# Performance work log

Measured on AMD Instinct MI355X. Metric: run time of the kernel, lower is better.

Reference implementation:

```python
import math
import jax, jax.numpy as jnp
import numpy as np

FS = 96000.0
N_BIQUADS = 16
HPF_FREQ_RANGE = (20.0, 500.0)
LPF_FREQ_RANGE = (5000.0, 20000.0)
SHELF_FREQ_RANGE = (50.0, 16000.0)
PEAK_FREQ_RANGE = (100.0, 15000.0)
Q_RANGE = (0.5, 16.0)
GAIN_RANGE = (-24.0, 24.0)
BROADBAND_RANGE = (-60.0, 0.0)


def _denorm_log(norm, lo, hi):
    return jnp.exp(math.log(lo) + norm * (math.log(hi) - math.log(lo)))


def _coef_highpass(fc, Q):
    w0 = 2.0 * math.pi * fc / FS
    alpha = jnp.sin(w0) / (2.0 * Q)
    c = jnp.cos(w0)
    b0 = (1 + c) / 2; b1 = -(1 + c); b2 = (1 + c) / 2
    a0 = 1 + alpha; a1 = -2 * c; a2 = 1 - alpha
    return b0 / a0, b1 / a0, b2 / a0, a1 / a0, a2 / a0


def _coef_lowpass(fc, Q):
    w0 = 2.0 * math.pi * fc / FS
    alpha = jnp.sin(w0) / (2.0 * Q)
    c = jnp.cos(w0)
    b0 = (1 - c) / 2; b1 = 1 - c; b2 = (1 - c) / 2
    a0 = 1 + alpha; a1 = -2 * c; a2 = 1 - alpha
    return b0 / a0, b1 / a0, b2 / a0, a1 / a0, a2 / a0


def _coef_lowshelf(fc, gain_db, Q):
    A = 10.0 ** (gain_db / 40.0)
    w0 = 2.0 * math.pi * fc / FS
    alpha = jnp.sin(w0) / (2.0 * Q)
    c = jnp.cos(w0)
    sA = jnp.sqrt(A)
    b0 = A * (A + 1 - (A - 1) * c + 2 * sA * alpha)
    b1 = 2 * A * (A - 1 - (A + 1) * c)
    b2 = A * (A + 1 - (A - 1) * c - 2 * sA * alpha)
    a0 = A + 1 + (A - 1) * c + 2 * sA * alpha
    a1 = -2 * (A - 1 + (A + 1) * c)
    a2 = A + 1 + (A - 1) * c - 2 * sA * alpha
    return b0 / a0, b1 / a0, b2 / a0, a1 / a0, a2 / a0


def _coef_highshelf(fc, gain_db, Q):
    A = 10.0 ** (gain_db / 40.0)
    w0 = 2.0 * math.pi * fc / FS
    alpha = jnp.sin(w0) / (2.0 * Q)
    c = jnp.cos(w0)
    sA = jnp.sqrt(A)
    b0 = A * (A + 1 + (A - 1) * c + 2 * sA * alpha)
    b1 = -2 * A * (A - 1 + (A + 1) * c)
    b2 = A * (A + 1 + (A - 1) * c - 2 * sA * alpha)
    a0 = A + 1 - (A - 1) * c + 2 * sA * alpha
    a1 = 2 * (A - 1 - (A + 1) * c)
    a2 = A + 1 - (A - 1) * c - 2 * sA * alpha
    return b0 / a0, b1 / a0, b2 / a0, a1 / a0, a2 / a0


def _coef_peak(fc, gain_db, Q):
    A = 10.0 ** (gain_db / 40.0)
    w0 = 2.0 * math.pi * fc / FS
    alpha = jnp.sin(w0) / (2.0 * Q)
    c = jnp.cos(w0)
    b0 = 1 + alpha * A; b1 = -2 * c; b2 = 1 - alpha * A
    a0 = 1 + alpha / A; a1 = -2 * c; a2 = 1 - alpha / A
    return b0 / a0, b1 / a0, b2 / a0, a1 / a0, a2 / a0


def _biquad(x, coefs):
    # x: (B, T); coefs: 5 arrays of shape (B,)
    b0, b1, b2, a1, a2 = coefs

    def step(carry, xt):  # xt: (B,)
        s1, s2 = carry
        y = b0 * xt + s1
        return (b1 * xt - a1 * y + s2, b2 * xt - a2 * y), y

    z = jnp.zeros(x.shape[0], x.dtype)
    _, ys = jax.lax.scan(step, (z, z), x.T)  # ys: (T, B)
    return ys.T


def _chain(audio, params):
    B = audio.shape[0]
    bp = params[:, :N_BIQUADS * 3].reshape(B, N_BIQUADS, 3)
    bb_lo, bb_hi = BROADBAND_RANGE
    in_db = bb_lo + params[:, -2] * (bb_hi - bb_lo)
    out_db = bb_lo + params[:, -1] * (bb_hi - bb_lo)
    x = audio * (10.0 ** (in_db / 20.0))[:, None]

    for i in range(N_BIQUADS):
        fn, gn, qn = bp[:, i, 0], bp[:, i, 1], bp[:, i, 2]
        Q = _denorm_log(qn, *Q_RANGE)
        gain = GAIN_RANGE[0] + gn * (GAIN_RANGE[1] - GAIN_RANGE[0])
        if i == 0:  # HPF
            coefs = _coef_highpass(_denorm_log(fn, *HPF_FREQ_RANGE), Q)
        elif i == 15:  # LPF
            coefs = _coef_lowpass(_denorm_log(fn, *LPF_FREQ_RANGE), Q)
        elif i == 1:  # low shelf
            coefs = _coef_lowshelf(_denorm_log(fn, *SHELF_FREQ_RANGE), gain, Q)
        elif i == 14:  # high shelf
            coefs = _coef_highshelf(_denorm_log(fn, *SHELF_FREQ_RANGE), gain, Q)
        else:  # peaking EQ
            coefs = _coef_peak(_denorm_log(fn, *PEAK_FREQ_RANGE), gain, Q)
        x = _biquad(x, coefs)

    return x * (10.0 ** (out_db / 20.0))[:, None]


def setup_inputs() -> dict:
    key = jax.random.key(0)
    k1, k2 = jax.random.split(key)
    audio = jax.random.normal(k1, (16, 262144), dtype=jnp.float32)
    params = jax.random.uniform(k2, (16, 50), dtype=jnp.float32)
    return {"audio": audio, "params": params}


def reference(audio, params):
    return _chain(audio, params)
```

## Files before the change

kernel.cpp:

```cpp
#include <hip/hip_runtime.h>
#include <math.h>

#define BATCH   16
#define T_LEN   262144
#define NB      16
#define L       64
#define GRP     64
#define SUB     16
#define CHAINS  4
#define NSUB    256
#define NSUP    16
#define NG      64
#define NCHUNK  4096

#define DPI 3.14159265358979323846264338327950288

#define OFF_COEF   0
#define OFF_A64    1536
#define OFF_A1K    17920
#define OFF_A16K   34304
#define OFF_QEND   50688
#define OFF_QSUP   181760
#define OFF_SSUP   189952
#define OFF_SARR   198144
#define OFF_P      329216

__device__ inline void stage_coefs(int i, double fn, double gn, double qn,
                                   double& B0, double& B1, double& B2,
                                   double& A1, double& A2) {
    const double FS = 96000.0;
    double Q    = exp(log(0.5) + qn * (log(16.0) - log(0.5)));
    double gain = -24.0 + gn * 48.0;
    double lo, hi;
    if (i == 0)            { lo = 20.0;   hi = 500.0;   }
    else if (i == 15)      { lo = 5000.0; hi = 20000.0; }
    else if (i == 1 || i == 14) { lo = 50.0; hi = 16000.0; }
    else                   { lo = 100.0;  hi = 15000.0; }
    double fc    = exp(log(lo) + fn * (log(hi) - log(lo)));
    double w0    = 2.0 * DPI * fc / FS;
    double alpha = sin(w0) / (2.0 * Q);
    double c     = cos(w0);
    double b0, b1, b2, a0, a1, a2;
    if (i == 0) {
        b0 = (1.0 + c) * 0.5; b1 = -(1.0 + c); b2 = (1.0 + c) * 0.5;
        a0 = 1.0 + alpha; a1 = -2.0 * c; a2 = 1.0 - alpha;
    } else if (i == 15) {
        b0 = (1.0 - c) * 0.5; b1 = 1.0 - c; b2 = (1.0 - c) * 0.5;
        a0 = 1.0 + alpha; a1 = -2.0 * c; a2 = 1.0 - alpha;
    } else if (i == 1) {
        double A = pow(10.0, gain / 40.0), sA = sqrt(A);
        b0 = A * ((A + 1.0) - (A - 1.0) * c + 2.0 * sA * alpha);
        b1 = 2.0 * A * ((A - 1.0) - (A + 1.0) * c);
        b2 = A * ((A + 1.0) - (A - 1.0) * c - 2.0 * sA * alpha);
        a0 = (A + 1.0) + (A - 1.0) * c + 2.0 * sA * alpha;
        a1 = -2.0 * ((A - 1.0) + (A + 1.0) * c);
        a2 = (A + 1.0) + (A - 1.0) * c - 2.0 * sA * alpha;
    } else if (i == 14) {
        double A = pow(10.0, gain / 40.0), sA = sqrt(A);
        b0 = A * ((A + 1.0) + (A - 1.0) * c + 2.0 * sA * alpha);
        b1 = -2.0 * A * ((A - 1.0) + (A + 1.0) * c);
        b2 = A * ((A + 1.0) + (A - 1.0) * c - 2.0 * sA * alpha);
        a0 = (A + 1.0) - (A - 1.0) * c + 2.0 * sA * alpha;
        a1 = 2.0 * ((A - 1.0) - (A + 1.0) * c);
        a2 = (A + 1.0) - (A - 1.0) * c - 2.0 * sA * alpha;
    } else {
        double A = pow(10.0, gain / 40.0);
        b0 = 1.0 + alpha * A; b1 = -2.0 * c; b2 = 1.0 - alpha * A;
        a0 = 1.0 + alpha / A; a1 = -2.0 * c; a2 = 1.0 - alpha / A;
    }
    B0 = b0 / a0; B1 = b1 / a0; B2 = b2 / a0; A1 = a1 / a0; A2 = a2 / a0;
}

__global__ __launch_bounds__(256) void k0_setup(const float* __restrict__ params,
                                                float* __restrict__ coefs,
                                                float* __restrict__ A64,
                                                float* __restrict__ A1K,
                                                float* __restrict__ A16K) {
    int b = blockIdx.x;
    int t = threadIdx.x;
    __shared__ double cf[NB][5];
    __shared__ double M1[32 * 32];
    __shared__ double M2[32 * 32];

    if (t < NB) {
        double B0, B1, B2, A1, A2;
        stage_coefs(t, (double)params[b * 50 + t * 3 + 0],
                       (double)params[b * 50 + t * 3 + 1],
                       (double)params[b * 50 + t * 3 + 2], B0, B1, B2, A1, A2);
        float f0 = (float)B0, f1 = (float)B1, f2 = (float)B2, f3 = (float)A1, f4 = (float)A2;
        cf[t][0] = (double)f0; cf[t][1] = (double)f1; cf[t][2] = (double)f2;
        cf[t][3] = (double)f3; cf[t][4] = (double)f4;
        float* cp = coefs + b * 96 + t * 5;
        cp[0] = f0; cp[1] = f1; cp[2] = f2; cp[3] = f3; cp[4] = f4;
    }
    if (t == NB) {
        double indb = -60.0 + (double)params[b * 50 + 48] * 60.0;
        coefs[b * 96 + 80] = (float)pow(10.0, indb / 20.0);
    }
    if (t == NB + 1) {
        double outdb = -60.0 + (double)params[b * 50 + 49] * 60.0;
        coefs[b * 96 + 81] = (float)pow(10.0, outdb / 20.0);
    }
    __syncthreads();

    if (t < 32) {
        double s1[NB], s2[NB];
#pragma unroll
        for (int i = 0; i < NB; i++) {
            s1[i] = (t == 2 * i) ? 1.0 : 0.0;
            s2[i] = (t == 2 * i + 1) ? 1.0 : 0.0;
        }
        double u = 0.0;
#pragma unroll
        for (int i = 0; i < NB; i++) {
            double y  = cf[i][0] * u + s1[i];
            double n1 = cf[i][1] * u - cf[i][3] * y + s2[i];
            double n2 = cf[i][2] * u - cf[i][4] * y;
            s1[i] = n1; s2[i] = n2; u = y;
        }
#pragma unroll
        for (int i = 0; i < NB; i++) {
            M1[(2 * i) * 32 + t]     = s1[i];
            M1[(2 * i + 1) * 32 + t] = s2[i];
        }
    }
    __syncthreads();

    int c  = t & 31;
    int r0 = t >> 5;
    double* src = M1;
    double* dst = M2;
    for (int sq = 0; sq < 14; sq++) {
        double acc[4] = {0.0, 0.0, 0.0, 0.0};
        for (int k = 0; k < 32; k++) {
            double bv = src[k * 32 + c];
#pragma unroll
            for (int e = 0; e < 4; e++)
                acc[e] += src[(e * 8 + r0) * 32 + k] * bv;
        }
#pragma unroll
        for (int e = 0; e < 4; e++) dst[(e * 8 + r0) * 32 + c] = acc[e];
        __syncthreads();
        { double* tmp = src; src = dst; dst = tmp; }
        float* out_m = (sq == 5) ? A64 : (sq == 9) ? A1K : (sq == 13) ? A16K : nullptr;
        if (out_m) {
#pragma unroll
            for (int e = 0; e < 4; e++) {
                int idx = (e * 8 + r0) * 32 + c;
                out_m[b * 1024 + idx] = (float)src[idx];
            }
        }
        __syncthreads();
    }
}

__global__ __launch_bounds__(64, 1) void k1_pass1(const float* __restrict__ audio,
                                                  const float* __restrict__ coefs,
                                                  const float* __restrict__ A64,
                                                  float* __restrict__ P,
                                                  float* __restrict__ Qend) {
    int blk   = blockIdx.x;
    int batch = blk >> 6;
    int grp   = blk & 63;
    int lane  = threadIdx.x;
    int chunk = grp * GRP + lane;

    const float* cf = coefs + batch * 96;
    float c0[NB], c1[NB], c2[NB], c3[NB], c4[NB];
#pragma unroll
    for (int i = 0; i < NB; i++) {
        c0[i] = cf[i * 5 + 0]; c1[i] = cf[i * 5 + 1]; c2[i] = cf[i * 5 + 2];
        c3[i] = cf[i * 5 + 3]; c4[i] = cf[i * 5 + 4];
    }
    float ing = cf[80];

    float s1[NB], s2[NB];
#pragma unroll
    for (int i = 0; i < NB; i++) { s1[i] = 0.f; s2[i] = 0.f; }

    const float4* xp = (const float4*)(audio + (size_t)batch * T_LEN + (size_t)chunk * L);
    float4 cur = xp[0];
    float4 nxt = xp[1];
#pragma unroll 1
    for (int tt = 0; tt < 16; tt++) {
        float4 fut = xp[(tt < 14) ? (tt + 2) : 15];
        float xs[4] = {cur.x, cur.y, cur.z, cur.w};
#pragma unroll
        for (int j = 0; j < 4; j++) {
            float u = ing * xs[j];
#pragma unroll
            for (int i = 0; i < NB; i++) {
                float y  = fmaf(c0[i], u, s1[i]);
                float n1 = fmaf(c1[i], u, s2[i]); n1 = fmaf(-c3[i], y, n1);
                float n2 = c2[i] * u;             n2 = fmaf(-c4[i], y, n2);
                s1[i] = n1; s2[i] = n2; u = y;
            }
        }
        cur = nxt; nxt = fut;
    }

    __shared__ float plds[GRP][33];
    float* pp = P + ((size_t)(batch * NCHUNK + chunk)) * 32;
#pragma unroll
    for (int i = 0; i < NB; i++) {
        float2 v; v.x = s1[i]; v.y = s2[i];
        *(float2*)(pp + 2 * i) = v;
        plds[lane][2 * i]     = s1[i];
        plds[lane][2 * i + 1] = s2[i];
    }
    __syncthreads();

    int row  = lane & 31;
    int half = lane >> 5;
    const float* alr = A64 + batch * 1024 + row * 32 + half * 16;
    float ar[16];
#pragma unroll
    for (int j = 0; j < 16; j++) ar[j] = alr[j];
    float q0 = 0.f, q1 = 0.f, q2 = 0.f, q3 = 0.f;
#pragma unroll 1
    for (int j = 0; j < SUB; j++) {
        float a0 = (half == 0) ? plds[0 * SUB + j][row] : 0.f;
        float a1 = (half == 0) ? plds[1 * SUB + j][row] : 0.f;
        float a2 = (half == 0) ? plds[2 * SUB + j][row] : 0.f;
        float a3 = (half == 0) ? plds[3 * SUB + j][row] : 0.f;
#pragma unroll
        for (int t = 0; t < 16; t++) {
            float w = ar[t];
            int src = half * 16 + t;
            a0 = fmaf(w, __shfl(q0, src, 64), a0);
            a1 = fmaf(w, __shfl(q1, src, 64), a1);
            a2 = fmaf(w, __shfl(q2, src, 64), a2);
            a3 = fmaf(w, __shfl(q3, src, 64), a3);
        }
        a0 += __shfl_xor(a0, 32, 64);
        a1 += __shfl_xor(a1, 32, 64);
        a2 += __shfl_xor(a2, 32, 64);
        a3 += __shfl_xor(a3, 32, 64);
        q0 = a0; q1 = a1; q2 = a2; q3 = a3;
    }
    if (lane < 32) {
        float* qe = Qend + ((size_t)(batch * NSUB + grp * CHAINS)) * 32 + row;
        qe[0 * 32] = q0; qe[1 * 32] = q1; qe[2 * 32] = q2; qe[3 * 32] = q3;
    }
}

__global__ __launch_bounds__(64, 1) void k2a(const float* __restrict__ A1K,
                                             const float* __restrict__ Qend,
                                             float* __restrict__ Qsup) {
    int batch = blockIdx.x >> 4;
    int sup   = blockIdx.x & 15;
    int lane  = threadIdx.x;
    int row   = lane & 31;
    int half  = lane >> 5;

    float pv[16];
#pragma unroll
    for (int j = 0; j < 16; j++)
        pv[j] = (half == 0) ? Qend[((size_t)(batch * NSUB + sup * 16 + j)) * 32 + row] : 0.f;

    const float* agr = A1K + batch * 1024 + row * 32 + half * 16;
    float ar[16];
#pragma unroll
    for (int j = 0; j < 16; j++) ar[j] = agr[j];

    float q = 0.f;
#pragma unroll 1
    for (int j = 0; j < 16; j++) {
        float acc = pv[j];
#pragma unroll
        for (int t = 0; t < 16; t++)
            acc = fmaf(ar[t], __shfl(q, half * 16 + t, 64), acc);
        acc += __shfl_xor(acc, 32, 64);
        q = acc;
    }
    if (lane < 32) Qsup[((size_t)(batch * NSUP + sup)) * 32 + row] = q;
}

__global__ __launch_bounds__(64, 1) void k2b(const float* __restrict__ A16K,
                                             const float* __restrict__ Qsup,
                                             float* __restrict__ Ssup) {
    int batch = blockIdx.x;
    int lane  = threadIdx.x;
    int row   = lane & 31;
    int half  = lane >> 5;

    float pv[16];
#pragma unroll
    for (int j = 0; j < 16; j++)
        pv[j] = (half == 0) ? Qsup[((size_t)(batch * NSUP + j)) * 32 + row] : 0.f;

    const float* agr = A16K + batch * 1024 + row * 32 + half * 16;
    float ar[16];
#pragma unroll
    for (int j = 0; j < 16; j++) ar[j] = agr[j];

    float S = 0.f;
#pragma unroll 1
    for (int s = 0; s < 16; s++) {
        if (lane < 32) Ssup[((size_t)(batch * NSUP + s)) * 32 + row] = S;
        float acc = pv[s];
#pragma unroll
        for (int t = 0; t < 16; t++)
            acc = fmaf(ar[t], __shfl(S, half * 16 + t, 64), acc);
        acc += __shfl_xor(acc, 32, 64);
        S = acc;
    }
}

__global__ __launch_bounds__(64, 1) void k2c(const float* __restrict__ A1K,
                                             const float* __restrict__ Qend,
                                             const float* __restrict__ Ssup,
                                             float* __restrict__ Sarr) {
    int batch = blockIdx.x >> 4;
    int sup   = blockIdx.x & 15;
    int lane  = threadIdx.x;
    int row   = lane & 31;
    int half  = lane >> 5;

    float pv[16];
#pragma unroll
    for (int j = 0; j < 16; j++)
        pv[j] = (half == 0) ? Qend[((size_t)(batch * NSUB + sup * 16 + j)) * 32 + row] : 0.f;

    const float* agr = A1K + batch * 1024 + row * 32 + half * 16;
    float ar[16];
#pragma unroll
    for (int j = 0; j < 16; j++) ar[j] = agr[j];

    float q = Ssup[((size_t)(batch * NSUP + sup)) * 32 + row];
#pragma unroll 1
    for (int j = 0; j < 16; j++) {
        if (lane < 32) Sarr[((size_t)(batch * NSUB + sup * 16 + j)) * 32 + row] = q;
        float acc = pv[j];
#pragma unroll
        for (int t = 0; t < 16; t++)
            acc = fmaf(ar[t], __shfl(q, half * 16 + t, 64), acc);
        acc += __shfl_xor(acc, 32, 64);
        q = acc;
    }
}

__global__ __launch_bounds__(64, 1) void k3_pass2(const float* __restrict__ audio,
                                                  const float* __restrict__ coefs,
                                                  const float* __restrict__ A64,
                                                  const float* __restrict__ P,
                                                  const float* __restrict__ Sarr,
                                                  float* __restrict__ out) {
    int blk   = blockIdx.x;
    int batch = blk >> 6;
    int grp   = blk & 63;
    int lane  = threadIdx.x;
    int chunk = grp * GRP + lane;

    __shared__ float plds[GRP][33];

    const float4* pp4 = (const float4*)(P + ((size_t)(batch * NCHUNK + chunk)) * 32);
#pragma unroll
    for (int r4 = 0; r4 < 8; r4++) {
        float4 v = pp4[r4];
        plds[lane][4 * r4 + 0] = v.x;
        plds[lane][4 * r4 + 1] = v.y;
        plds[lane][4 * r4 + 2] = v.z;
        plds[lane][4 * r4 + 3] = v.w;
    }
    __syncthreads();

    {
        int row  = lane & 31;
        int half = lane >> 5;
        const float* alr = A64 + batch * 1024 + row * 32 + half * 16;
        float ar[16];
#pragma unroll
        for (int j = 0; j < 16; j++) ar[j] = alr[j];
        const float* sp = Sarr + ((size_t)(batch * NSUB + grp * CHAINS)) * 32 + row;
        float q0 = sp[0 * 32], q1 = sp[1 * 32], q2 = sp[2 * 32], q3 = sp[3 * 32];
#pragma unroll 1
        for (int j = 0; j < SUB; j++) {
            float a0 = (half == 0) ? plds[0 * SUB + j][row] : 0.f;
            float a1 = (half == 0) ? plds[1 * SUB + j][row] : 0.f;
            float a2 = (half == 0) ? plds[2 * SUB + j][row] : 0.f;
            float a3 = (half == 0) ? plds[3 * SUB + j][row] : 0.f;
            if (half == 0) {
                plds[0 * SUB + j][row] = q0;
                plds[1 * SUB + j][row] = q1;
                plds[2 * SUB + j][row] = q2;
                plds[3 * SUB + j][row] = q3;
            }
#pragma unroll
            for (int t = 0; t < 16; t++) {
                float w = ar[t];
                int src = half * 16 + t;
                a0 = fmaf(w, __shfl(q0, src, 64), a0);
                a1 = fmaf(w, __shfl(q1, src, 64), a1);
                a2 = fmaf(w, __shfl(q2, src, 64), a2);
                a3 = fmaf(w, __shfl(q3, src, 64), a3);
            }
            a0 += __shfl_xor(a0, 32, 64);
            a1 += __shfl_xor(a1, 32, 64);
            a2 += __shfl_xor(a2, 32, 64);
            a3 += __shfl_xor(a3, 32, 64);
            q0 = a0; q1 = a1; q2 = a2; q3 = a3;
        }
    }
    __syncthreads();

    const float* cf = coefs + batch * 96;
    float c0[NB], c1[NB], c2[NB], c3[NB], c4[NB];
#pragma unroll
    for (int i = 0; i < NB; i++) {
        c0[i] = cf[i * 5 + 0]; c1[i] = cf[i * 5 + 1]; c2[i] = cf[i * 5 + 2];
        c3[i] = cf[i * 5 + 3]; c4[i] = cf[i * 5 + 4];
    }
    float ing  = cf[80];
    float outg = cf[81];

    float s1[NB], s2[NB];
#pragma unroll
    for (int i = 0; i < NB; i++) {
        s1[i] = plds[lane][2 * i];
        s2[i] = plds[lane][2 * i + 1];
    }

    const float4* xp = (const float4*)(audio + (size_t)batch * T_LEN + (size_t)chunk * L);
    float4* yp = (float4*)(out + (size_t)batch * T_LEN + (size_t)chunk * L);
    float4 cur = xp[0];
    float4 nxt = xp[1];
#pragma unroll 1
    for (int tt = 0; tt < 16; tt++) {
        float4 fut = xp[(tt < 14) ? (tt + 2) : 15];
        float xs[4] = {cur.x, cur.y, cur.z, cur.w};
        float ys[4];
#pragma unroll
        for (int j = 0; j < 4; j++) {
            float u = ing * xs[j];
#pragma unroll
            for (int i = 0; i < NB; i++) {
                float y  = fmaf(c0[i], u, s1[i]);
                float n1 = fmaf(c1[i], u, s2[i]); n1 = fmaf(-c3[i], y, n1);
                float n2 = c2[i] * u;             n2 = fmaf(-c4[i], y, n2);
                s1[i] = n1; s2[i] = n2; u = y;
            }
            ys[j] = outg * u;
        }
        float4 yv; yv.x = ys[0]; yv.y = ys[1]; yv.z = ys[2]; yv.w = ys[3];
        yp[tt] = yv;
        cur = nxt; nxt = fut;
    }
}

extern "C" void kernel_launch(void* const* d_in, const int* in_sizes, int n_in,
                              void* d_out, int out_size, void* d_ws, size_t ws_size,
                              hipStream_t stream) {
    const float* audio  = (const float*)d_in[0];
    const float* params = (const float*)d_in[1];
    float* out = (float*)d_out;
    float* ws  = (float*)d_ws;

    float* coefs = ws + OFF_COEF;
    float* A64   = ws + OFF_A64;
    float* A1K   = ws + OFF_A1K;
    float* A16K  = ws + OFF_A16K;
    float* Qend  = ws + OFF_QEND;
    float* Qsup  = ws + OFF_QSUP;
    float* Ssup  = ws + OFF_SSUP;
    float* Sarr  = ws + OFF_SARR;
    float* P     = ws + OFF_P;

    k0_setup<<<BATCH, 256, 0, stream>>>(params, coefs, A64, A1K, A16K);
    k1_pass1<<<BATCH * NG, 64, 0, stream>>>(audio, coefs, A64, P, Qend);
    k2a<<<BATCH * NSUP, 64, 0, stream>>>(A1K, Qend, Qsup);
    k2b<<<BATCH, 64, 0, stream>>>(A16K, Qsup, Ssup);
    k2c<<<BATCH * NSUP, 64, 0, stream>>>(A1K, Qend, Ssup, Sarr);
    k3_pass2<<<BATCH * NG, 64, 0, stream>>>(audio, coefs, A64, P, Sarr, out);
}
```

Before: 159.5 us.

## Fuse scan kernels into one cooperative kernel with grid syncs

Replaces the five post-setup kernels (pass1, three carry-propagation kernels, pass2) with a single cooperative kernel that uses grid.sync between phases. Per-chunk partial states stay in shared memory instead of going to a global P buffer, and the coefficients and A64 matrix are loaded once. This removes several kernel launch gaps and the P store/reload traffic. The cost is four grid-wide barriers, idle blocks during the small serial phases, and a requirement that all 1024 blocks be co-resident.

```diff
diff --git a/kernel.cpp b/kernel.cpp
--- a/kernel.cpp
+++ b/kernel.cpp
@@ -1,5 +1,8 @@
 #include <hip/hip_runtime.h>
+#include <hip/hip_cooperative_groups.h>
 #include <math.h>
+
+namespace cg = cooperative_groups;
 
 #define BATCH   16
 #define T_LEN   262144
@@ -15,15 +18,14 @@
 
 #define DPI 3.14159265358979323846264338327950288
 
-#define OFF_COEF   0
-#define OFF_A64    1536
-#define OFF_A1K    17920
-#define OFF_A16K   34304
-#define OFF_QEND   50688
-#define OFF_QSUP   181760
-#define OFF_SSUP   189952
-#define OFF_SARR   198144
-#define OFF_P      329216
+#define OFF_COEF  0
+#define OFF_A64   1536
+#define OFF_A1K   17920
+#define OFF_A16K  34304
+#define OFF_QEND  50688
+#define OFF_QSUP  181760
+#define OFF_SSUP  189952
+#define OFF_SARR  198144
 
 __device__ inline void stage_coefs(int i, double fn, double gn, double qn,
                                    double& B0, double& B1, double& B2,
@@ -154,16 +156,35 @@
     }
 }
 
-__global__ __launch_bounds__(64, 1) void k1_pass1(const float* __restrict__ audio,
-                                                  const float* __restrict__ coefs,
-                                                  const float* __restrict__ A64,
-                                                  float* __restrict__ P,
-                                                  float* __restrict__ Qend) {
+__device__ __forceinline__ float mv_step(const float* ar, float q, float addv, int half) {
+    float acc = addv;
+#pragma unroll
+    for (int t = 0; t < 16; t++)
+        acc = fmaf(ar[t], __shfl(q, half * 16 + t, 64), acc);
+    acc += __shfl_xor(acc, 32, 64);
+    return acc;
+}
+
+__global__ __launch_bounds__(64, 1) void mega(const float* __restrict__ audio,
+                                              const float* __restrict__ coefs,
+                                              const float* __restrict__ A64,
+                                              const float* __restrict__ A1K,
+                                              const float* __restrict__ A16K,
+                                              float* __restrict__ Qend,
+                                              float* __restrict__ Qsup,
+                                              float* __restrict__ Ssup,
+                                              float* __restrict__ Sarr,
+                                              float* __restrict__ out) {
+    cg::grid_group grid = cg::this_grid();
     int blk   = blockIdx.x;
     int batch = blk >> 6;
     int grp   = blk & 63;
     int lane  = threadIdx.x;
     int chunk = grp * GRP + lane;
+    int row   = lane & 31;
+    int half  = lane >> 5;
+
+    __shared__ float plds[GRP][33];
 
     const float* cf = coefs + batch * 96;
     float c0[NB], c1[NB], c2[NB], c3[NB], c4[NB];
@@ -172,208 +193,138 @@
         c0[i] = cf[i * 5 + 0]; c1[i] = cf[i * 5 + 1]; c2[i] = cf[i * 5 + 2];
         c3[i] = cf[i * 5 + 3]; c4[i] = cf[i * 5 + 4];
     }
-    float ing = cf[80];
-
-    float s1[NB], s2[NB];
-#pragma unroll
-    for (int i = 0; i < NB; i++) { s1[i] = 0.f; s2[i] = 0.f; }
-
-    const float4* xp = (const float4*)(audio + (size_t)batch * T_LEN + (size_t)chunk * L);
-    float4 cur = xp[0];
-    float4 nxt = xp[1];
-#pragma unroll 1
-    for (int tt = 0; tt < 16; tt++) {
-        float4 fut = xp[(tt < 14) ? (tt + 2) : 15];
-        float xs[4] = {cur.x, cur.y, cur.z, cur.w};
-#pragma unroll
-        for (int j = 0; j < 4; j++) {
-            float u = ing * xs[j];
-#pragma unroll
-            for (int i = 0; i < NB; i++) {
-                float y  = fmaf(c0[i], u, s1[i]);
-                float n1 = fmaf(c1[i], u, s2[i]); n1 = fmaf(-c3[i], y, n1);
-                float n2 = c2[i] * u;             n2 = fmaf(-c4[i], y, n2);
-                s1[i] = n1; s2[i] = n2; u = y;
-            }
-        }
-        cur = nxt; nxt = fut;
-    }
-
-    __shared__ float plds[GRP][33];
-    float* pp = P + ((size_t)(batch * NCHUNK + chunk)) * 32;
-#pragma unroll
-    for (int i = 0; i < NB; i++) {
-        float2 v; v.x = s1[i]; v.y = s2[i];
-        *(float2*)(pp + 2 * i) = v;
-        plds[lane][2 * i]     = s1[i];
-        plds[lane][2 * i + 1] = s2[i];
+    float ing  = cf[80];
+    float outg = cf[81];
+
+    float ar64[16];
+    {
+        const float* ap = A64 + batch * 1024 + row * 32 + half * 16;
+#pragma unroll
+        for (int j = 0; j < 16; j++) ar64[j] = ap[j];
+    }
+
+    {
+        float s1[NB], s2[NB];
+#pragma unroll
+        for (int i = 0; i < NB; i++) { s1[i] = 0.f; s2[i] = 0.f; }
+        const float4* xp = (const float4*)(audio + (size_t)batch * T_LEN + (size_t)chunk * L);
+        float4 a0v = xp[0];
+        float4 a1v = xp[1];
+#pragma unroll 1
+        for (int tt = 0; tt < 16; tt++) {
+            float4 fut = xp[(tt < 14) ? (tt + 2) : 15];
+            float xs[4] = {a0v.x, a0v.y, a0v.z, a0v.w};
+#pragma unroll
+            for (int j = 0; j < 4; j++) {
+                float u = ing * xs[j];
+#pragma unroll
+                for (int i = 0; i < NB; i++) {
+                    float y  = fmaf(c0[i], u, s1[i]);
+                    float n1 = fmaf(c1[i], u, s2[i]); n1 = fmaf(-c3[i], y, n1);
+                    float n2 = c2[i] * u;             n2 = fmaf(-c4[i], y, n2);
+                    s1[i] = n1; s2[i] = n2; u = y;
+                }
+            }
+            a0v = a1v; a1v = fut;
+        }
+#pragma unroll
+        for (int i = 0; i < NB; i++) {
+            plds[lane][2 * i]     = s1[i];
+            plds[lane][2 * i + 1] = s2[i];
+        }
     }
     __syncthreads();
-
-    int row  = lane & 31;
-    int half = lane >> 5;
-    const float* alr = A64 + batch * 1024 + row * 32 + half * 16;
-    float ar[16];
-#pragma unroll
-    for (int j = 0; j < 16; j++) ar[j] = alr[j];
-    float q0 = 0.f, q1 = 0.f, q2 = 0.f, q3 = 0.f;
-#pragma unroll 1
-    for (int j = 0; j < SUB; j++) {
-        float a0 = (half == 0) ? plds[0 * SUB + j][row] : 0.f;
-        float a1 = (half == 0) ? plds[1 * SUB + j][row] : 0.f;
-        float a2 = (half == 0) ? plds[2 * SUB + j][row] : 0.f;
-        float a3 = (half == 0) ? plds[3 * SUB + j][row] : 0.f;
-#pragma unroll
-        for (int t = 0; t < 16; t++) {
-            float w = ar[t];
-            int src = half * 16 + t;
-            a0 = fmaf(w, __shfl(q0, src, 64), a0);
-            a1 = fmaf(w, __shfl(q1, src, 64), a1);
-            a2 = fmaf(w, __shfl(q2, src, 64), a2);
-            a3 = fmaf(w, __shfl(q3, src, 64), a3);
-        }
-        a0 += __shfl_xor(a0, 32, 64);
-        a1 += __shfl_xor(a1, 32, 64);
-        a2 += __shfl_xor(a2, 32, 64);
-        a3 += __shfl_xor(a3, 32, 64);
-        q0 = a0; q1 = a1; q2 = a2; q3 = a3;
-    }
-    if (lane < 32) {
-        float* qe = Qend + ((size_t)(batch * NSUB + grp * CHAINS)) * 32 + row;
-        qe[0 * 32] = q0; qe[1 * 32] = q1; qe[2 * 32] = q2; qe[3 * 32] = q3;
-    }
-}
-
-__global__ __launch_bounds__(64, 1) void k2a(const float* __restrict__ A1K,
-                                             const float* __restrict__ Qend,
-                                             float* __restrict__ Qsup) {
-    int batch = blockIdx.x >> 4;
-    int sup   = blockIdx.x & 15;
-    int lane  = threadIdx.x;
-    int row   = lane & 31;
-    int half  = lane >> 5;
-
-    float pv[16];
-#pragma unroll
-    for (int j = 0; j < 16; j++)
-        pv[j] = (half == 0) ? Qend[((size_t)(batch * NSUB + sup * 16 + j)) * 32 + row] : 0.f;
-
-    const float* agr = A1K + batch * 1024 + row * 32 + half * 16;
-    float ar[16];
-#pragma unroll
-    for (int j = 0; j < 16; j++) ar[j] = agr[j];
-
-    float q = 0.f;
-#pragma unroll 1
-    for (int j = 0; j < 16; j++) {
-        float acc = pv[j];
-#pragma unroll
-        for (int t = 0; t < 16; t++)
-            acc = fmaf(ar[t], __shfl(q, half * 16 + t, 64), acc);
-        acc += __shfl_xor(acc, 32, 64);
-        q = acc;
-    }
-    if (lane < 32) Qsup[((size_t)(batch * NSUP + sup)) * 32 + row] = q;
-}
-
-__global__ __launch_bounds__(64, 1) void k2b(const float* __restrict__ A16K,
-                                             const float* __restrict__ Qsup,
-                                             float* __restrict__ Ssup) {
-    int batch = blockIdx.x;
-    int lane  = threadIdx.x;
-    int row   = lane & 31;
-    int half  = lane >> 5;
-
-    float pv[16];
-#pragma unroll
-    for (int j = 0; j < 16; j++)
-        pv[j] = (half == 0) ? Qsup[((size_t)(batch * NSUP + j)) * 32 + row] : 0.f;
-
-    const float* agr = A16K + batch * 1024 + row * 32 + half * 16;
-    float ar[16];
-#pragma unroll
-    for (int j = 0; j < 16; j++) ar[j] = agr[j];
-
-    float S = 0.f;
-#pragma unroll 1
-    for (int s = 0; s < 16; s++) {
-        if (lane < 32) Ssup[((size_t)(batch * NSUP + s)) * 32 + row] = S;
-        float acc = pv[s];
-#pragma unroll
-        for (int t = 0; t < 16; t++)
-            acc = fmaf(ar[t], __shfl(S, half * 16 + t, 64), acc);
-        acc += __shfl_xor(acc, 32, 64);
-        S = acc;
-    }
-}
-
-__global__ __launch_bounds__(64, 1) void k2c(const float* __restrict__ A1K,
-                                             const float* __restrict__ Qend,
-                                             const float* __restrict__ Ssup,
-                                             float* __restrict__ Sarr) {
-    int batch = blockIdx.x >> 4;
-    int sup   = blockIdx.x & 15;
-    int lane  = threadIdx.x;
-    int row   = lane & 31;
-    int half  = lane >> 5;
-
-    float pv[16];
-#pragma unroll
-    for (int j = 0; j < 16; j++)
-        pv[j] = (half == 0) ? Qend[((size_t)(batch * NSUB + sup * 16 + j)) * 32 + row] : 0.f;
-
-    const float* agr = A1K + batch * 1024 + row * 32 + half * 16;
-    float ar[16];
-#pragma unroll
-    for (int j = 0; j < 16; j++) ar[j] = agr[j];
-
-    float q = Ssup[((size_t)(batch * NSUP + sup)) * 32 + row];
-#pragma unroll 1
-    for (int j = 0; j < 16; j++) {
-        if (lane < 32) Sarr[((size_t)(batch * NSUB + sup * 16 + j)) * 32 + row] = q;
-        float acc = pv[j];
-#pragma unroll
-        for (int t = 0; t < 16; t++)
-            acc = fmaf(ar[t], __shfl(q, half * 16 + t, 64), acc);
-        acc += __shfl_xor(acc, 32, 64);
-        q = acc;
-    }
-}
-
-__global__ __launch_bounds__(64, 1) void k3_pass2(const float* __restrict__ audio,
-                                                  const float* __restrict__ coefs,
-                                                  const float* __restrict__ A64,
-                                                  const float* __restrict__ P,
-                                                  const float* __restrict__ Sarr,
-                                                  float* __restrict__ out) {
-    int blk   = blockIdx.x;
-    int batch = blk >> 6;
-    int grp   = blk & 63;
-    int lane  = threadIdx.x;
-    int chunk = grp * GRP + lane;
-
-    __shared__ float plds[GRP][33];
-
-    const float4* pp4 = (const float4*)(P + ((size_t)(batch * NCHUNK + chunk)) * 32);
-#pragma unroll
-    for (int r4 = 0; r4 < 8; r4++) {
-        float4 v = pp4[r4];
-        plds[lane][4 * r4 + 0] = v.x;
-        plds[lane][4 * r4 + 1] = v.y;
-        plds[lane][4 * r4 + 2] = v.z;
-        plds[lane][4 * r4 + 3] = v.w;
-    }
-    __syncthreads();
-
     {
-        int row  = lane & 31;
-        int half = lane >> 5;
-        const float* alr = A64 + batch * 1024 + row * 32 + half * 16;
-        float ar[16];
-#pragma unroll
-        for (int j = 0; j < 16; j++) ar[j] = alr[j];
+        float q0 = 0.f, q1 = 0.f, q2 = 0.f, q3 = 0.f;
+#pragma unroll 1
+        for (int j = 0; j < SUB; j++) {
+            float a0 = (half == 0) ? plds[0 * SUB + j][row] : 0.f;
+            float a1 = (half == 0) ? plds[1 * SUB + j][row] : 0.f;
+            float a2 = (half == 0) ? plds[2 * SUB + j][row] : 0.f;
+            float a3 = (half == 0) ? plds[3 * SUB + j][row] : 0.f;
+#pragma unroll
+            for (int t = 0; t < 16; t++) {
+                float w = ar64[t];
+                int src = half * 16 + t;
+                a0 = fmaf(w, __shfl(q0, src, 64), a0);
+                a1 = fmaf(w, __shfl(q1, src, 64), a1);
+                a2 = fmaf(w, __shfl(q2, src, 64), a2);
+                a3 = fmaf(w, __shfl(q3, src, 64), a3);
+            }
+            a0 += __shfl_xor(a0, 32, 64);
+            a1 += __shfl_xor(a1, 32, 64);
+            a2 += __shfl_xor(a2, 32, 64);
+            a3 += __shfl_xor(a3, 32, 64);
+            q0 = a0; q1 = a1; q2 = a2; q3 = a3;
+        }
+        if (lane < 32) {
+            float* qe = Qend + ((size_t)(batch * NSUB + grp * CHAINS)) * 32 + row;
+            qe[0] = q0; qe[32] = q1; qe[64] = q2; qe[96] = q3;
+        }
+    }
+
+    __threadfence();
+    grid.sync();
+
+    float ar1k[16];
+    if (grp < 16) {
+        int sup = grp;
+        const float* ap = A1K + batch * 1024 + row * 32 + half * 16;
+#pragma unroll
+        for (int j = 0; j < 16; j++) ar1k[j] = ap[j];
+        float pv[16];
+#pragma unroll
+        for (int j = 0; j < 16; j++)
+            pv[j] = (half == 0) ? Qend[((size_t)(batch * NSUB + sup * 16 + j)) * 32 + row] : 0.f;
+        float q = 0.f;
+#pragma unroll 1
+        for (int j = 0; j < 16; j++) q = mv_step(ar1k, q, pv[j], half);
+        if (lane < 32) Qsup[((size_t)(batch * NSUP + sup)) * 32 + row] = q;
+    }
+
+    __threadfence();
+    grid.sync();
+
+    if (grp == 0) {
+        float ark[16];
+        const float* ap = A16K + batch * 1024 + row * 32 + half * 16;
+#pragma unroll
+        for (int j = 0; j < 16; j++) ark[j] = ap[j];
+        float pv[16];
+#pragma unroll
+        for (int j = 0; j < 16; j++)
+            pv[j] = (half == 0) ? Qsup[((size_t)(batch * NSUP + j)) * 32 + row] : 0.f;
+        float S = 0.f;
+#pragma unroll 1
+        for (int s = 0; s < 16; s++) {
+            if (lane < 32) Ssup[((size_t)(batch * NSUP + s)) * 32 + row] = S;
+            S = mv_step(ark, S, pv[s], half);
+        }
+    }
+
+    __threadfence();
+    grid.sync();
+
+    if (grp < 16) {
+        int sup = grp;
+        float pv[16];
+#pragma unroll
+        for (int j = 0; j < 16; j++)
+            pv[j] = (half == 0) ? Qend[((size_t)(batch * NSUB + sup * 16 + j)) * 32 + row] : 0.f;
+        float q = Ssup[((size_t)(batch * NSUP + sup)) * 32 + row];
+#pragma unroll 1
+        for (int j = 0; j < 16; j++) {
+            if (lane < 32) Sarr[((size_t)(batch * NSUB + sup * 16 + j)) * 32 + row] = q;
+            q = mv_step(ar1k, q, pv[j], half);
+        }
+    }
+
+    __threadfence();
+    grid.sync();
+
+    {
         const float* sp = Sarr + ((size_t)(batch * NSUB + grp * CHAINS)) * 32 + row;
-        float q0 = sp[0 * 32], q1 = sp[1 * 32], q2 = sp[2 * 32], q3 = sp[3 * 32];
+        float q0 = sp[0], q1 = sp[32], q2 = sp[64], q3 = sp[96];
 #pragma unroll 1
         for (int j = 0; j < SUB; j++) {
             float a0 = (half == 0) ? plds[0 * SUB + j][row] : 0.f;
@@ -388,7 +339,7 @@
             }
 #pragma unroll
             for (int t = 0; t < 16; t++) {
-                float w = ar[t];
+                float w = ar64[t];
                 int src = half * 16 + t;
                 a0 = fmaf(w, __shfl(q0, src, 64), a0);
                 a1 = fmaf(w, __shfl(q1, src, 64), a1);
@@ -404,47 +355,38 @@
     }
     __syncthreads();
 
-    const float* cf = coefs + batch * 96;
-    float c0[NB], c1[NB], c2[NB], c3[NB], c4[NB];
-#pragma unroll
-    for (int i = 0; i < NB; i++) {
-        c0[i] = cf[i * 5 + 0]; c1[i] = cf[i * 5 + 1]; c2[i] = cf[i * 5 + 2];
-        c3[i] = cf[i * 5 + 3]; c4[i] = cf[i * 5 + 4];
-    }
-    float ing  = cf[80];
-    float outg = cf[81];
-
-    float s1[NB], s2[NB];
-#pragma unroll
-    for (int i = 0; i < NB; i++) {
-        s1[i] = plds[lane][2 * i];
-        s2[i] = plds[lane][2 * i + 1];
-    }
-
-    const float4* xp = (const float4*)(audio + (size_t)batch * T_LEN + (size_t)chunk * L);
-    float4* yp = (float4*)(out + (size_t)batch * T_LEN + (size_t)chunk * L);
-    float4 cur = xp[0];
-    float4 nxt = xp[1];
-#pragma unroll 1
-    for (int tt = 0; tt < 16; tt++) {
-        float4 fut = xp[(tt < 14) ? (tt + 2) : 15];
-        float xs[4] = {cur.x, cur.y, cur.z, cur.w};
-        float ys[4];
-#pragma unroll
-        for (int j = 0; j < 4; j++) {
-            float u = ing * xs[j];
-#pragma unroll
-            for (int i = 0; i < NB; i++) {
-                float y  = fmaf(c0[i], u, s1[i]);
-                float n1 = fmaf(c1[i], u, s2[i]); n1 = fmaf(-c3[i], y, n1);
-                float n2 = c2[i] * u;             n2 = fmaf(-c4[i], y, n2);
-                s1[i] = n1; s2[i] = n2; u = y;
-            }
-            ys[j] = outg * u;
-        }
-        float4 yv; yv.x = ys[0]; yv.y = ys[1]; yv.z = ys[2]; yv.w = ys[3];
-        yp[tt] = yv;
-        cur = nxt; nxt = fut;
+    {
+        float s1[NB], s2[NB];
+#pragma unroll
+        for (int i = 0; i < NB; i++) {
+            s1[i] = plds[lane][2 * i];
+            s2[i] = plds[lane][2 * i + 1];
+        }
+        const float4* xp = (const float4*)(audio + (size_t)batch * T_LEN + (size_t)chunk * L);
+        float4* yp = (float4*)(out + (size_t)batch * T_LEN + (size_t)chunk * L);
+        float4 a0v = xp[0];
+        float4 a1v = xp[1];
+#pragma unroll 1
+        for (int tt = 0; tt < 16; tt++) {
+            float4 fut = xp[(tt < 14) ? (tt + 2) : 15];
+            float xs[4] = {a0v.x, a0v.y, a0v.z, a0v.w};
+            float ys[4];
+#pragma unroll
+            for (int j = 0; j < 4; j++) {
+                float u = ing * xs[j];
+#pragma unroll
+                for (int i = 0; i < NB; i++) {
+                    float y  = fmaf(c0[i], u, s1[i]);
+                    float n1 = fmaf(c1[i], u, s2[i]); n1 = fmaf(-c3[i], y, n1);
+                    float n2 = c2[i] * u;             n2 = fmaf(-c4[i], y, n2);
+                    s1[i] = n1; s2[i] = n2; u = y;
+                }
+                ys[j] = outg * u;
+            }
+            float4 yv; yv.x = ys[0]; yv.y = ys[1]; yv.z = ys[2]; yv.w = ys[3];
+            yp[tt] = yv;
+            a0v = a1v; a1v = fut;
+        }
     }
 }
 
@@ -464,12 +406,16 @@
     float* Qsup  = ws + OFF_QSUP;
     float* Ssup  = ws + OFF_SSUP;
     float* Sarr  = ws + OFF_SARR;
-    float* P     = ws + OFF_P;
 
     k0_setup<<<BATCH, 256, 0, stream>>>(params, coefs, A64, A1K, A16K);
-    k1_pass1<<<BATCH * NG, 64, 0, stream>>>(audio, coefs, A64, P, Qend);
-    k2a<<<BATCH * NSUP, 64, 0, stream>>>(A1K, Qend, Qsup);
-    k2b<<<BATCH, 64, 0, stream>>>(A16K, Qsup, Ssup);
-    k2c<<<BATCH * NSUP, 64, 0, stream>>>(A1K, Qend, Ssup, Sarr);
-    k3_pass2<<<BATCH * NG, 64, 0, stream>>>(audio, coefs, A64, P, Sarr, out);
+
+    const float* c_coefs = coefs;
+    const float* c_A64   = A64;
+    const float* c_A1K   = A1K;
+    const float* c_A16K  = A16K;
+    void* args[] = {(void*)&audio, (void*)&c_coefs, (void*)&c_A64, (void*)&c_A1K,
+                    (void*)&c_A16K, (void*)&Qend, (void*)&Qsup, (void*)&Ssup,
+                    (void*)&Sarr, (void*)&out};
+    hipLaunchCooperativeKernel((const void*)mega, dim3(BATCH * NG), dim3(64),
+                               args, 0, stream);
 }
```

Measured after the change: 626.3 us. 293% more time.

## Fuse three state-combine kernels into one block per batch and coalesce P layout

Applied to the files above, without the earlier changes.

Replaces the three small combine kernels (k2a, k2b, k2c) with one 256-thread kernel per batch. Each of its four waves handles four superchunk chains, exchanging intermediate states through shared memory with block barriers, which removes two kernel launches and their global round trips. The per-chunk state buffer P is also changed to a lane-contiguous layout so stores in pass1 and loads in pass2 are coalesced. In exchange, the combine step now runs on only 16 blocks with more serial work per wave instead of 256 parallel blocks.

```diff
diff --git a/kernel.cpp b/kernel.cpp
--- a/kernel.cpp
+++ b/kernel.cpp
@@ -15,15 +15,13 @@
 
 #define DPI 3.14159265358979323846264338327950288
 
-#define OFF_COEF   0
-#define OFF_A64    1536
-#define OFF_A1K    17920
-#define OFF_A16K   34304
-#define OFF_QEND   50688
-#define OFF_QSUP   181760
-#define OFF_SSUP   189952
-#define OFF_SARR   198144
-#define OFF_P      329216
+#define OFF_COEF  0
+#define OFF_A64   1536
+#define OFF_A1K   17920
+#define OFF_A16K  34304
+#define OFF_QEND  50688
+#define OFF_SARR  181760
+#define OFF_P     312832
 
 __device__ inline void stage_coefs(int i, double fn, double gn, double qn,
                                    double& B0, double& B1, double& B2,
@@ -154,6 +152,15 @@
     }
 }
 
+__device__ __forceinline__ float mv_step(const float* ar, float q, float addv, int half) {
+    float acc = addv;
+#pragma unroll
+    for (int t = 0; t < 16; t++)
+        acc = fmaf(ar[t], __shfl(q, half * 16 + t, 64), acc);
+    acc += __shfl_xor(acc, 32, 64);
+    return acc;
+}
+
 __global__ __launch_bounds__(64, 1) void k1_pass1(const float* __restrict__ audio,
                                                   const float* __restrict__ coefs,
                                                   const float* __restrict__ A64,
@@ -199,12 +206,18 @@
         cur = nxt; nxt = fut;
     }
 
+    {
+        float* pb = P + ((size_t)(batch * NG + grp)) * 2048;
+#pragma unroll
+        for (int i = 0; i < NB; i++) {
+            pb[(2 * i) * 64 + lane]     = s1[i];
+            pb[(2 * i + 1) * 64 + lane] = s2[i];
+        }
+    }
+
     __shared__ float plds[GRP][33];
-    float* pp = P + ((size_t)(batch * NCHUNK + chunk)) * 32;
 #pragma unroll
     for (int i = 0; i < NB; i++) {
-        float2 v; v.x = s1[i]; v.y = s2[i];
-        *(float2*)(pp + 2 * i) = v;
         plds[lane][2 * i]     = s1[i];
         plds[lane][2 * i + 1] = s2[i];
     }
@@ -240,103 +253,116 @@
     }
     if (lane < 32) {
         float* qe = Qend + ((size_t)(batch * NSUB + grp * CHAINS)) * 32 + row;
-        qe[0 * 32] = q0; qe[1 * 32] = q1; qe[2 * 32] = q2; qe[3 * 32] = q3;
-    }
-}
-
-__global__ __launch_bounds__(64, 1) void k2a(const float* __restrict__ A1K,
-                                             const float* __restrict__ Qend,
-                                             float* __restrict__ Qsup) {
-    int batch = blockIdx.x >> 4;
-    int sup   = blockIdx.x & 15;
-    int lane  = threadIdx.x;
+        qe[0] = q0; qe[32] = q1; qe[64] = q2; qe[96] = q3;
+    }
+}
+
+__global__ __launch_bounds__(256, 1) void k2_combine(const float* __restrict__ A1K,
+                                                     const float* __restrict__ A16K,
+                                                     const float* __restrict__ Qend,
+                                                     float* __restrict__ Sarr) {
+    int batch = blockIdx.x;
+    int tid   = threadIdx.x;
+    int wave  = tid >> 6;
+    int lane  = tid & 63;
     int row   = lane & 31;
     int half  = lane >> 5;
 
-    float pv[16];
-#pragma unroll
-    for (int j = 0; j < 16; j++)
-        pv[j] = (half == 0) ? Qend[((size_t)(batch * NSUB + sup * 16 + j)) * 32 + row] : 0.f;
-
-    const float* agr = A1K + batch * 1024 + row * 32 + half * 16;
-    float ar[16];
-#pragma unroll
-    for (int j = 0; j < 16; j++) ar[j] = agr[j];
-
-    float q = 0.f;
-#pragma unroll 1
-    for (int j = 0; j < 16; j++) {
-        float acc = pv[j];
-#pragma unroll
-        for (int t = 0; t < 16; t++)
-            acc = fmaf(ar[t], __shfl(q, half * 16 + t, 64), acc);
-        acc += __shfl_xor(acc, 32, 64);
-        q = acc;
-    }
-    if (lane < 32) Qsup[((size_t)(batch * NSUP + sup)) * 32 + row] = q;
-}
-
-__global__ __launch_bounds__(64, 1) void k2b(const float* __restrict__ A16K,
-                                             const float* __restrict__ Qsup,
-                                             float* __restrict__ Ssup) {
-    int batch = blockIdx.x;
-    int lane  = threadIdx.x;
-    int row   = lane & 31;
-    int half  = lane >> 5;
-
-    float pv[16];
-#pragma unroll
-    for (int j = 0; j < 16; j++)
-        pv[j] = (half == 0) ? Qsup[((size_t)(batch * NSUP + j)) * 32 + row] : 0.f;
-
-    const float* agr = A16K + batch * 1024 + row * 32 + half * 16;
-    float ar[16];
-#pragma unroll
-    for (int j = 0; j < 16; j++) ar[j] = agr[j];
-
-    float S = 0.f;
-#pragma unroll 1
-    for (int s = 0; s < 16; s++) {
-        if (lane < 32) Ssup[((size_t)(batch * NSUP + s)) * 32 + row] = S;
-        float acc = pv[s];
-#pragma unroll
-        for (int t = 0; t < 16; t++)
-            acc = fmaf(ar[t], __shfl(S, half * 16 + t, 64), acc);
-        acc += __shfl_xor(acc, 32, 64);
-        S = acc;
-    }
-}
-
-__global__ __launch_bounds__(64, 1) void k2c(const float* __restrict__ A1K,
-                                             const float* __restrict__ Qend,
-                                             const float* __restrict__ Ssup,
-                                             float* __restrict__ Sarr) {
-    int batch = blockIdx.x >> 4;
-    int sup   = blockIdx.x & 15;
-    int lane  = threadIdx.x;
-    int row   = lane & 31;
-    int half  = lane >> 5;
-
-    float pv[16];
-#pragma unroll
-    for (int j = 0; j < 16; j++)
-        pv[j] = (half == 0) ? Qend[((size_t)(batch * NSUB + sup * 16 + j)) * 32 + row] : 0.f;
-
-    const float* agr = A1K + batch * 1024 + row * 32 + half * 16;
-    float ar[16];
-#pragma unroll
-    for (int j = 0; j < 16; j++) ar[j] = agr[j];
-
-    float q = Ssup[((size_t)(batch * NSUP + sup)) * 32 + row];
-#pragma unroll 1
-    for (int j = 0; j < 16; j++) {
-        if (lane < 32) Sarr[((size_t)(batch * NSUB + sup * 16 + j)) * 32 + row] = q;
-        float acc = pv[j];
-#pragma unroll
-        for (int t = 0; t < 16; t++)
-            acc = fmaf(ar[t], __shfl(q, half * 16 + t, 64), acc);
-        acc += __shfl_xor(acc, 32, 64);
-        q = acc;
+    __shared__ float qe[NSUB][32];
+    __shared__ float qs[NSUP][32];
+    __shared__ float ss[NSUP][32];
+
+    {
+        const float4* src4 = (const float4*)(Qend + (size_t)batch * NSUB * 32);
+        float4* dst4 = (float4*)&qe[0][0];
+        for (int i = tid; i < NSUB * 32 / 4; i += 256) dst4[i] = src4[i];
+    }
+    float ar1k[16];
+    {
+        const float* ap = A1K + batch * 1024 + row * 32 + half * 16;
+#pragma unroll
+        for (int j = 0; j < 16; j++) ar1k[j] = ap[j];
+    }
+    __syncthreads();
+
+    int s0i = wave * 4;
+    {
+        float q0 = 0.f, q1 = 0.f, q2 = 0.f, q3 = 0.f;
+#pragma unroll 1
+        for (int j = 0; j < 16; j++) {
+            float a0 = (half == 0) ? qe[(s0i + 0) * 16 + j][row] : 0.f;
+            float a1 = (half == 0) ? qe[(s0i + 1) * 16 + j][row] : 0.f;
+            float a2 = (half == 0) ? qe[(s0i + 2) * 16 + j][row] : 0.f;
+            float a3 = (half == 0) ? qe[(s0i + 3) * 16 + j][row] : 0.f;
+#pragma unroll
+            for (int t = 0; t < 16; t++) {
+                float w = ar1k[t];
+                int src = half * 16 + t;
+                a0 = fmaf(w, __shfl(q0, src, 64), a0);
+                a1 = fmaf(w, __shfl(q1, src, 64), a1);
+                a2 = fmaf(w, __shfl(q2, src, 64), a2);
+                a3 = fmaf(w, __shfl(q3, src, 64), a3);
+            }
+            a0 += __shfl_xor(a0, 32, 64);
+            a1 += __shfl_xor(a1, 32, 64);
+            a2 += __shfl_xor(a2, 32, 64);
+            a3 += __shfl_xor(a3, 32, 64);
+            q0 = a0; q1 = a1; q2 = a2; q3 = a3;
+        }
+        if (lane < 32) {
+            qs[s0i + 0][row] = q0; qs[s0i + 1][row] = q1;
+            qs[s0i + 2][row] = q2; qs[s0i + 3][row] = q3;
+        }
+    }
+    __syncthreads();
+
+    if (wave == 0) {
+        float ark[16];
+        const float* ap = A16K + batch * 1024 + row * 32 + half * 16;
+#pragma unroll
+        for (int j = 0; j < 16; j++) ark[j] = ap[j];
+        float S = 0.f;
+#pragma unroll 1
+        for (int s = 0; s < 16; s++) {
+            if (lane < 32) ss[s][row] = S;
+            float addv = (half == 0) ? qs[s][row] : 0.f;
+            S = mv_step(ark, S, addv, half);
+        }
+    }
+    __syncthreads();
+
+    {
+        float q0 = ss[s0i + 0][row];
+        float q1 = ss[s0i + 1][row];
+        float q2 = ss[s0i + 2][row];
+        float q3 = ss[s0i + 3][row];
+#pragma unroll 1
+        for (int j = 0; j < 16; j++) {
+            if (lane < 32) {
+                Sarr[((size_t)(batch * NSUB + (s0i + 0) * 16 + j)) * 32 + row] = q0;
+                Sarr[((size_t)(batch * NSUB + (s0i + 1) * 16 + j)) * 32 + row] = q1;
+                Sarr[((size_t)(batch * NSUB + (s0i + 2) * 16 + j)) * 32 + row] = q2;
+                Sarr[((size_t)(batch * NSUB + (s0i + 3) * 16 + j)) * 32 + row] = q3;
+            }
+            float a0 = (half == 0) ? qe[(s0i + 0) * 16 + j][row] : 0.f;
+            float a1 = (half == 0) ? qe[(s0i + 1) * 16 + j][row] : 0.f;
+            float a2 = (half == 0) ? qe[(s0i + 2) * 16 + j][row] : 0.f;
+            float a3 = (half == 0) ? qe[(s0i + 3) * 16 + j][row] : 0.f;
+#pragma unroll
+            for (int t = 0; t < 16; t++) {
+                float w = ar1k[t];
+                int src = half * 16 + t;
+                a0 = fmaf(w, __shfl(q0, src, 64), a0);
+                a1 = fmaf(w, __shfl(q1, src, 64), a1);
+                a2 = fmaf(w, __shfl(q2, src, 64), a2);
+                a3 = fmaf(w, __shfl(q3, src, 64), a3);
+            }
+            a0 += __shfl_xor(a0, 32, 64);
+            a1 += __shfl_xor(a1, 32, 64);
+            a2 += __shfl_xor(a2, 32, 64);
+            a3 += __shfl_xor(a3, 32, 64);
+            q0 = a0; q1 = a1; q2 = a2; q3 = a3;
+        }
     }
 }
 
@@ -351,29 +377,28 @@
     int grp   = blk & 63;
     int lane  = threadIdx.x;
     int chunk = grp * GRP + lane;
+    int row   = lane & 31;
+    int half  = lane >> 5;
 
     __shared__ float plds[GRP][33];
 
-    const float4* pp4 = (const float4*)(P + ((size_t)(batch * NCHUNK + chunk)) * 32);
-#pragma unroll
-    for (int r4 = 0; r4 < 8; r4++) {
-        float4 v = pp4[r4];
-        plds[lane][4 * r4 + 0] = v.x;
-        plds[lane][4 * r4 + 1] = v.y;
-        plds[lane][4 * r4 + 2] = v.z;
-        plds[lane][4 * r4 + 3] = v.w;
-    }
-    __syncthreads();
-
-    {
-        int row  = lane & 31;
-        int half = lane >> 5;
+    {
+        const float* pb = P + ((size_t)(batch * NG + grp)) * 2048;
+        float pv[32];
+#pragma unroll
+        for (int s = 0; s < 32; s++) pv[s] = pb[s * 64 + lane];
+#pragma unroll
+        for (int s = 0; s < 32; s++) plds[lane][s] = pv[s];
+    }
+    __syncthreads();
+
+    {
         const float* alr = A64 + batch * 1024 + row * 32 + half * 16;
         float ar[16];
 #pragma unroll
         for (int j = 0; j < 16; j++) ar[j] = alr[j];
         const float* sp = Sarr + ((size_t)(batch * NSUB + grp * CHAINS)) * 32 + row;
-        float q0 = sp[0 * 32], q1 = sp[1 * 32], q2 = sp[2 * 32], q3 = sp[3 * 32];
+        float q0 = sp[0], q1 = sp[32], q2 = sp[64], q3 = sp[96];
 #pragma unroll 1
         for (int j = 0; j < SUB; j++) {
             float a0 = (half == 0) ? plds[0 * SUB + j][row] : 0.f;
@@ -461,15 +486,11 @@
     float* A1K   = ws + OFF_A1K;
     float* A16K  = ws + OFF_A16K;
     float* Qend  = ws + OFF_QEND;
-    float* Qsup  = ws + OFF_QSUP;
-    float* Ssup  = ws + OFF_SSUP;
     float* Sarr  = ws + OFF_SARR;
     float* P     = ws + OFF_P;
 
     k0_setup<<<BATCH, 256, 0, stream>>>(params, coefs, A64, A1K, A16K);
     k1_pass1<<<BATCH * NG, 64, 0, stream>>>(audio, coefs, A64, P, Qend);
-    k2a<<<BATCH * NSUP, 64, 0, stream>>>(A1K, Qend, Qsup);
-    k2b<<<BATCH, 64, 0, stream>>>(A16K, Qsup, Ssup);
-    k2c<<<BATCH * NSUP, 64, 0, stream>>>(A1K, Qend, Ssup, Sarr);
+    k2_combine<<<BATCH, 256, 0, stream>>>(A1K, A16K, Qend, Sarr);
     k3_pass2<<<BATCH * NG, 64, 0, stream>>>(audio, coefs, A64, P, Sarr, out);
 }
```

Measured after the change: 173.0 us. +8.5%, slower.
